# Kernel tuning notes

Measured on AMD Instinct MI355X. Metric: run time of the kernel, lower is better.

The kernel has to match this reference:

```python
import jax, jax.numpy as jnp
import numpy as np


def setup_inputs() -> dict:
    key = jax.random.key(0)
    k1, k2 = jax.random.split(key)
    B, T, D, K = 8, 4096, 256, 1024
    z = jax.random.normal(k1, (B, T, D), dtype=jnp.float32)
    codebook = jax.random.uniform(k2, (K, D), dtype=jnp.float32)
    return {"z": z, "codebook": codebook}


def reference(z, codebook):
    # Squared L2 distance via dot-product decomposition (same argmin as
    # the broadcasted squared-difference in the original module, without
    # materializing the (B,T,K,D) intermediate).
    #   ||z - c||^2 = ||z||^2 - 2 z.c + ||c||^2
    z_sq = jnp.sum(z * z, axis=-1, keepdims=True)            # (B,T,1)
    c_sq = jnp.sum(codebook * codebook, axis=-1)             # (K,)
    cross = jnp.einsum("btd,kd->btk", z, codebook)           # (B,T,K)
    l2_distance = z_sq - 2.0 * cross + c_sq                  # (B,T,K)
    codebook_indices = jnp.argmin(l2_distance, axis=-1)      # (B,T)
    z_q = codebook[codebook_indices]                         # (B,T,D)
    # Straight-through estimator
    z_q = z + jax.lax.stop_gradient(z_q - z)
    return (z_q, codebook_indices)
```

## Files before the change

kernel.cpp:

```cpp
#include <hip/hip_runtime.h>
#include <math.h>

#define NTOK   32768
#define NDIM   256
#define NCODE  1024
#define NSTRIP 8
#define CHUNK  (128 * 32)

typedef _Float16 f16x8 __attribute__((ext_vector_type(8)));
typedef float    f32x4 __attribute__((ext_vector_type(4)));

__device__ __forceinline__ void gld_lds16(const void* g, void* l) {
    __builtin_amdgcn_global_load_lds(
        (const __attribute__((address_space(1))) void*)g,
        (__attribute__((address_space(3))) void*)l, 16, 0, 0);
}

__global__ __launch_bounds__(256) void prep_cb(
        const float* __restrict__ cb,
        _Float16* __restrict__ ch, _Float16* __restrict__ cl,
        float* __restrict__ csq) {
    const int L   = blockIdx.x * 256 + threadIdx.x;
    const int row = L >> 5;
    const int g   = L & 31;

    const float* src = cb + (size_t)row * NDIM + g * 8;
    float4 a0 = *(const float4*)src;
    float4 a1 = *(const float4*)(src + 4);
    float v[8] = {a0.x, a0.y, a0.z, a0.w, a1.x, a1.y, a1.z, a1.w};
    f16x8 hi, lo;
    float s = 0.f;
    #pragma unroll
    for (int e = 0; e < 8; ++e) {
        _Float16 h = (_Float16)v[e];
        hi[e] = h;
        lo[e] = (_Float16)(v[e] - (float)h);
        s += v[e] * v[e];
    }
    const size_t dst = (size_t)((row >> 7) * 8 + (g >> 2)) * CHUNK
                     + (row & 127) * 32 + (g & 3) * 8;
    *(f16x8*)&ch[dst] = hi;
    *(f16x8*)&cl[dst] = lo;
    #pragma unroll
    for (int off = 16; off > 0; off >>= 1) s += __shfl_down(s, off, 32);
    if ((threadIdx.x & 31) == 0) csq[row] = s;
}

__global__ __launch_bounds__(256, 2) void vq_main(
        const float* __restrict__ z,
        const _Float16* __restrict__ ch, const _Float16* __restrict__ cl,
        const float* __restrict__ csq, const float* __restrict__ cb,
        float* __restrict__ zq, float* __restrict__ io) {
    __shared__ _Float16 Bh[4 * CHUNK];
    __shared__ _Float16 Bl[4 * CHUNK];

    const int tid  = threadIdx.x;
    const int w    = tid >> 6;
    const int lane = tid & 63;
    const int quad = lane >> 4, lr = lane & 15;
    const int m0   = blockIdx.x * 64;

    f16x8 ah[8], al[8];
    {
        const float* zp = z + (size_t)(m0 + w * 16 + lr) * NDIM + quad * 8;
        #pragma unroll
        for (int c = 0; c < 8; ++c) {
            float4 a0 = *(const float4*)(zp + c * 32);
            float4 a1 = *(const float4*)(zp + c * 32 + 4);
            float v[8] = {a0.x, a0.y, a0.z, a0.w, a1.x, a1.y, a1.z, a1.w};
            #pragma unroll
            for (int e = 0; e < 8; ++e) {
                _Float16 h = (_Float16)v[e];
                ah[c][e] = h;
                al[c][e] = (_Float16)(v[e] - (float)h);
            }
        }
    }

    float bv[4];
    int   bi[4];
    #pragma unroll
    for (int r = 0; r < 4; ++r) { bv[r] = INFINITY; bi[r] = 0x7fffffff; }

    f32x4 acc[8];
    #pragma unroll
    for (int nt = 0; nt < 8; ++nt) acc[nt] = (f32x4){0.f, 0.f, 0.f, 0.f};

    for (int strip = 0; strip < NSTRIP; ++strip) {
        float cs[8];
        #pragma unroll
        for (int nt = 0; nt < 8; ++nt)
            cs[nt] = csq[strip * 128 + nt * 16 + lr];

        #pragma unroll
        for (int kh = 0; kh < 2; ++kh) {
            __syncthreads();
            {
                const size_t base = (size_t)(strip * 8 + kh * 4) * CHUNK
                                  + w * CHUNK + lane * 8;
                const _Float16* sh = ch + base;
                const _Float16* sl = cl + base;
                #pragma unroll
                for (int i = 0; i < 8; ++i) {
                    gld_lds16(sh + i * 512, Bh + w * CHUNK + i * 512);
                    gld_lds16(sl + i * 512, Bl + w * CHUNK + i * 512);
                }
            }
            __syncthreads();

            #pragma unroll
            for (int k4 = 0; k4 < 4; ++k4) {
                const int kg = kh * 4 + k4;
                f16x8 fbh[8], fbl[8];
                #pragma unroll
                for (int nt = 0; nt < 8; ++nt) {
                    const int off = k4 * CHUNK + (nt * 16 + lr) * 32 + quad * 8;
                    fbh[nt] = *(const f16x8*)&Bh[off];
                    fbl[nt] = *(const f16x8*)&Bl[off];
                }
                #pragma unroll
                for (int nt = 0; nt < 8; ++nt) {
                    acc[nt] = __builtin_amdgcn_mfma_f32_16x16x32_f16(
                                  ah[kg], fbh[nt], acc[nt], 0, 0, 0);
                    acc[nt] = __builtin_amdgcn_mfma_f32_16x16x32_f16(
                                  al[kg], fbh[nt], acc[nt], 0, 0, 0);
                    acc[nt] = __builtin_amdgcn_mfma_f32_16x16x32_f16(
                                  ah[kg], fbl[nt], acc[nt], 0, 0, 0);
                }
            }
        }

        #pragma unroll
        for (int r = 0; r < 4; ++r)
            #pragma unroll
            for (int nt = 0; nt < 8; ++nt) {
                float v = cs[nt] - 2.0f * acc[nt][r];
                int   n = strip * 128 + nt * 16 + lr;
                if (v < bv[r] || (v == bv[r] && n < bi[r])) { bv[r] = v; bi[r] = n; }
            }
        #pragma unroll
        for (int nt = 0; nt < 8; ++nt) acc[nt] = (f32x4){0.f, 0.f, 0.f, 0.f};
    }

    #pragma unroll
    for (int msk = 1; msk < 16; msk <<= 1)
        #pragma unroll
        for (int r = 0; r < 4; ++r) {
            float ov = __shfl_xor(bv[r], msk, 64);
            int   oi = __shfl_xor(bi[r], msk, 64);
            if (ov < bv[r] || (ov == bv[r] && oi < bi[r])) { bv[r] = ov; bi[r] = oi; }
        }

    __syncthreads();
    int* bestS = (int*)Bh;
    if (lr == 0) {
        #pragma unroll
        for (int r = 0; r < 4; ++r) {
            int row = w * 16 + quad * 4 + r;
            bestS[row] = bi[r];
            io[m0 + row] = (float)bi[r];
        }
    }
    __syncthreads();

    const int tr = tid >> 4, tc = tid & 15;
    #pragma unroll
    for (int p = 0; p < 4; ++p) {
        int row = p * 16 + tr;
        const float* src = cb + (size_t)bestS[row] * NDIM;
        float*       dst = zq + (size_t)(m0 + row) * NDIM;
        #pragma unroll
        for (int q = 0; q < 4; ++q) {
            int col = q * 64 + tc * 4;
            *(float4*)&dst[col] = *(const float4*)&src[col];
        }
    }
}

extern "C" void kernel_launch(void* const* d_in, const int* in_sizes, int n_in,
                              void* d_out, int out_size, void* d_ws, size_t ws_size,
                              hipStream_t stream) {
    const float* z  = (const float*)d_in[0];
    const float* cb = (const float*)d_in[1];

    float* zq = (float*)d_out;
    float* io = (float*)d_out + (size_t)NTOK * NDIM;

    _Float16* ch  = (_Float16*)d_ws;
    _Float16* cl  = ch + (size_t)NCODE * NDIM;
    float*    csq = (float*)(cl + (size_t)NCODE * NDIM);

    prep_cb<<<NCODE * 32 / 256, 256, 0, stream>>>(cb, ch, cl, csq);

    vq_main<<<NTOK / 64, 256, 0, stream>>>(z, ch, cl, csq, cb, zq, io);
}
```

Baseline: 139.7 us.

## Split waves into 2x2 M/N tiling to halve LDS B-fragment reads

Each wave now computes a 32-row by 64-code sub-tile (two M tiles, four N tiles) instead of 16 rows by 128 codes. Each B fragment loaded from LDS is reused across two A tiles, which halves per-wave LDS read traffic. The cost is double the A-fragment registers per wave. It also needs an extra cross-wave argmin merge through shared memory plus one more barrier. With launch_bounds(256,2), the higher register pressure could cause spills.

```diff
diff --git a/kernel.cpp b/kernel.cpp
--- a/kernel.cpp
+++ b/kernel.cpp
@@ -58,11 +58,14 @@
     const int w    = tid >> 6;
     const int lane = tid & 63;
     const int quad = lane >> 4, lr = lane & 15;
+    const int my   = w >> 1, nx = w & 1;
     const int m0   = blockIdx.x * 64;
 
-    f16x8 ah[8], al[8];
-    {
-        const float* zp = z + (size_t)(m0 + w * 16 + lr) * NDIM + quad * 8;
+    f16x8 ah[2][8], al[2][8];
+    #pragma unroll
+    for (int mt = 0; mt < 2; ++mt) {
+        const float* zp = z + (size_t)(m0 + my * 32 + mt * 16 + lr) * NDIM
+                        + quad * 8;
         #pragma unroll
         for (int c = 0; c < 8; ++c) {
             float4 a0 = *(const float4*)(zp + c * 32);
@@ -71,33 +74,37 @@
             #pragma unroll
             for (int e = 0; e < 8; ++e) {
                 _Float16 h = (_Float16)v[e];
-                ah[c][e] = h;
-                al[c][e] = (_Float16)(v[e] - (float)h);
+                ah[mt][c][e] = h;
+                al[mt][c][e] = (_Float16)(v[e] - (float)h);
             }
         }
     }
 
-    float bv[4];
-    int   bi[4];
-    #pragma unroll
-    for (int r = 0; r < 4; ++r) { bv[r] = INFINITY; bi[r] = 0x7fffffff; }
-
-    f32x4 acc[8];
-    #pragma unroll
-    for (int nt = 0; nt < 8; ++nt) acc[nt] = (f32x4){0.f, 0.f, 0.f, 0.f};
+    float bv[2][4];
+    int   bi[2][4];
+    #pragma unroll
+    for (int mt = 0; mt < 2; ++mt)
+        #pragma unroll
+        for (int r = 0; r < 4; ++r) { bv[mt][r] = INFINITY; bi[mt][r] = 0x7fffffff; }
+
+    f32x4 acc[2][4];
+    #pragma unroll
+    for (int mt = 0; mt < 2; ++mt)
+        #pragma unroll
+        for (int t = 0; t < 4; ++t) acc[mt][t] = (f32x4){0.f, 0.f, 0.f, 0.f};
 
     for (int strip = 0; strip < NSTRIP; ++strip) {
-        float cs[8];
-        #pragma unroll
-        for (int nt = 0; nt < 8; ++nt)
-            cs[nt] = csq[strip * 128 + nt * 16 + lr];
+        float cs[4];
+        #pragma unroll
+        for (int t = 0; t < 4; ++t)
+            cs[t] = csq[strip * 128 + (nx * 4 + t) * 16 + lr];
 
         #pragma unroll
         for (int kh = 0; kh < 2; ++kh) {
             __syncthreads();
             {
-                const size_t base = (size_t)(strip * 8 + kh * 4) * CHUNK
-                                  + w * CHUNK + lane * 8;
+                const size_t base = (size_t)(strip * 8 + kh * 4 + w) * CHUNK
+                                  + lane * 8;
                 const _Float16* sh = ch + base;
                 const _Float16* sl = cl + base;
                 #pragma unroll
@@ -111,55 +118,83 @@
             #pragma unroll
             for (int k4 = 0; k4 < 4; ++k4) {
                 const int kg = kh * 4 + k4;
-                f16x8 fbh[8], fbl[8];
-                #pragma unroll
-                for (int nt = 0; nt < 8; ++nt) {
-                    const int off = k4 * CHUNK + (nt * 16 + lr) * 32 + quad * 8;
-                    fbh[nt] = *(const f16x8*)&Bh[off];
-                    fbl[nt] = *(const f16x8*)&Bl[off];
-                }
-                #pragma unroll
-                for (int nt = 0; nt < 8; ++nt) {
-                    acc[nt] = __builtin_amdgcn_mfma_f32_16x16x32_f16(
-                                  ah[kg], fbh[nt], acc[nt], 0, 0, 0);
-                    acc[nt] = __builtin_amdgcn_mfma_f32_16x16x32_f16(
-                                  al[kg], fbh[nt], acc[nt], 0, 0, 0);
-                    acc[nt] = __builtin_amdgcn_mfma_f32_16x16x32_f16(
-                                  ah[kg], fbl[nt], acc[nt], 0, 0, 0);
-                }
+                f16x8 fbh[4], fbl[4];
+                #pragma unroll
+                for (int t = 0; t < 4; ++t) {
+                    const int off = k4 * CHUNK
+                                  + ((nx * 4 + t) * 16 + lr) * 32 + quad * 8;
+                    fbh[t] = *(const f16x8*)&Bh[off];
+                    fbl[t] = *(const f16x8*)&Bl[off];
+                }
+                #pragma unroll
+                for (int mt = 0; mt < 2; ++mt)
+                    #pragma unroll
+                    for (int t = 0; t < 4; ++t) {
+                        acc[mt][t] = __builtin_amdgcn_mfma_f32_16x16x32_f16(
+                                         ah[mt][kg], fbh[t], acc[mt][t], 0, 0, 0);
+                        acc[mt][t] = __builtin_amdgcn_mfma_f32_16x16x32_f16(
+                                         al[mt][kg], fbh[t], acc[mt][t], 0, 0, 0);
+                        acc[mt][t] = __builtin_amdgcn_mfma_f32_16x16x32_f16(
+                                         ah[mt][kg], fbl[t], acc[mt][t], 0, 0, 0);
+                    }
             }
         }
 
         #pragma unroll
-        for (int r = 0; r < 4; ++r)
-            #pragma unroll
-            for (int nt = 0; nt < 8; ++nt) {
-                float v = cs[nt] - 2.0f * acc[nt][r];
-                int   n = strip * 128 + nt * 16 + lr;
-                if (v < bv[r] || (v == bv[r] && n < bi[r])) { bv[r] = v; bi[r] = n; }
-            }
-        #pragma unroll
-        for (int nt = 0; nt < 8; ++nt) acc[nt] = (f32x4){0.f, 0.f, 0.f, 0.f};
+        for (int mt = 0; mt < 2; ++mt)
+            #pragma unroll
+            for (int r = 0; r < 4; ++r)
+                #pragma unroll
+                for (int t = 0; t < 4; ++t) {
+                    float v = cs[t] - 2.0f * acc[mt][t][r];
+                    int   n = strip * 128 + (nx * 4 + t) * 16 + lr;
+                    if (v < bv[mt][r] || (v == bv[mt][r] && n < bi[mt][r])) {
+                        bv[mt][r] = v; bi[mt][r] = n;
+                    }
+                }
+        #pragma unroll
+        for (int mt = 0; mt < 2; ++mt)
+            #pragma unroll
+            for (int t = 0; t < 4; ++t) acc[mt][t] = (f32x4){0.f, 0.f, 0.f, 0.f};
     }
 
     #pragma unroll
     for (int msk = 1; msk < 16; msk <<= 1)
         #pragma unroll
-        for (int r = 0; r < 4; ++r) {
-            float ov = __shfl_xor(bv[r], msk, 64);
-            int   oi = __shfl_xor(bi[r], msk, 64);
-            if (ov < bv[r] || (ov == bv[r] && oi < bi[r])) { bv[r] = ov; bi[r] = oi; }
-        }
+        for (int mt = 0; mt < 2; ++mt)
+            #pragma unroll
+            for (int r = 0; r < 4; ++r) {
+                float ov = __shfl_xor(bv[mt][r], msk, 64);
+                int   oi = __shfl_xor(bi[mt][r], msk, 64);
+                if (ov < bv[mt][r] || (ov == bv[mt][r] && oi < bi[mt][r])) {
+                    bv[mt][r] = ov; bi[mt][r] = oi;
+                }
+            }
 
     __syncthreads();
-    int* bestS = (int*)Bh;
+    float* sval  = (float*)Bh;
+    int*   sidx  = (int*)&Bh[512];
+    int*   bestS = (int*)&Bh[1024];
+
     if (lr == 0) {
         #pragma unroll
-        for (int r = 0; r < 4; ++r) {
-            int row = w * 16 + quad * 4 + r;
-            bestS[row] = bi[r];
-            io[m0 + row] = (float)bi[r];
-        }
+        for (int mt = 0; mt < 2; ++mt)
+            #pragma unroll
+            for (int r = 0; r < 4; ++r) {
+                int row = my * 32 + mt * 16 + quad * 4 + r;
+                sval[row * 2 + nx] = bv[mt][r];
+                sidx[row * 2 + nx] = bi[mt][r];
+            }
+    }
+    __syncthreads();
+
+    if (tid < 64) {
+        float v0 = sval[tid * 2], v1 = sval[tid * 2 + 1];
+        int   i0 = sidx[tid * 2], i1 = sidx[tid * 2 + 1];
+        bool take1 = (v1 < v0) || (v1 == v0 && i1 < i0);
+        int best = take1 ? i1 : i0;
+        bestS[tid] = best;
+        io[m0 + tid] = (float)best;
     }
     __syncthreads();
 
```

Result: faster. 133.0 us (-4.8%).
